# Optimization experiments

Hardware: AMD Instinct MI355X
Metric: run time of the kernel (lower is better)

The kernel has to match this reference:

```python
import jax, jax.numpy as jnp
import numpy as np

NUM_HEADS = 16


def setup_inputs() -> dict:
    key = jax.random.key(0)
    ks = jax.random.split(key, 4)
    B, C, T, D = 1, 1, 3072, 1024
    s = 1.0 / np.sqrt(D)
    return {
        "x": jax.random.normal(ks[0], (B, C, T, D), dtype=jnp.float32),
        "Wq": jax.random.normal(ks[1], (D, D), dtype=jnp.float32) * s,
        "bq": jnp.zeros((D,), dtype=jnp.float32),
        "Wk": jax.random.normal(ks[2], (D, D), dtype=jnp.float32) * s,
        "bk": jnp.zeros((D,), dtype=jnp.float32),
        "Wv": jax.random.normal(ks[3], (D, D), dtype=jnp.float32) * s,
        "bv": jnp.zeros((D,), dtype=jnp.float32),
        "gamma": jnp.float32(0.5),  # learned scalar; 0.0 at torch init, nonzero here for a meaningful signal
    }


def reference(x, Wq, bq, Wk, bk, Wv, bv, gamma):
    # x: (B, C, T, D); Linear acts on last dim (torch: y = x @ W.T + b)
    B, C, T, D = x.shape
    H = NUM_HEADS
    q = (jnp.einsum("bctd,ed->bcte", x, Wq) + bq).reshape(B, -1, T, H)  # (B, X, T, H), X = C*D/H
    k = (jnp.einsum("bctd,ed->bcte", x, Wk) + bk).reshape(B, -1, T, H)
    v = (jnp.einsum("bctd,ed->bcte", x, Wv) + bv).reshape(B, -1, T, H)
    q = q.transpose(0, 3, 2, 1)  # (B, H, T, X)
    k = k.transpose(0, 3, 1, 2)  # (B, H, X, T)
    energy = q @ k               # (B, H, T, T)  -- note: NO 1/sqrt(d) scaling, as in source
    attn = jax.nn.softmax(energy, axis=-1)
    v = v.transpose(0, 3, 2, 1)  # (B, H, T, X)
    out = attn @ v               # (B, H, T, X)
    out = out.transpose(0, 2, 3, 1).reshape(B, T, -1)  # (B, T, X*H) = (B, T, C*D)
    # residual broadcast: (B, T, C*D) + (B, C, T, D); valid since B == C == 1
    return gamma * out + x
```

## Files before the change

kernel.cpp:

```cpp
#include <hip/hip_runtime.h>


typedef _Float16 v8h __attribute__((ext_vector_type(8)));
typedef _Float16 v4h __attribute__((ext_vector_type(4)));
typedef __fp16   v2pk __attribute__((ext_vector_type(2)));
typedef __fp16   v4pk __attribute__((ext_vector_type(4)));
typedef float    v4f __attribute__((ext_vector_type(4)));

#define TSEQ 3072
#define DM   1024
#define NH   16
#define XD   64
#define LOG2E 1.44269504f

__device__ __forceinline__ void async_load16(const void* g, void* l) {
  __builtin_amdgcn_global_load_lds(
      (const __attribute__((address_space(1))) unsigned int*)g,
      (__attribute__((address_space(3))) unsigned int*)l,
      16, 0, 0);
}

__device__ __forceinline__ float fexp2(float x) {
  float r; asm("v_exp_f32 %0, %1" : "=v"(r) : "v"(x)); return r;
}
__device__ __forceinline__ float flog2(float x) {
  float r; asm("v_log_f32 %0, %1" : "=v"(r) : "v"(x)); return r;
}

extern "C" __global__ __launch_bounds__(256) void cvt_kernel(
    const float* __restrict__ x, const float* __restrict__ wq,
    const float* __restrict__ wk, const float* __restrict__ wv,
    _Float16* __restrict__ xb, _Float16* __restrict__ wb)
{
  const int NX4 = (TSEQ * DM) / 4;
  const int NT  = NX4 * 2;
  for (int i = blockIdx.x * blockDim.x + threadIdx.x; i < NT;
       i += gridDim.x * blockDim.x) {
    float4 v;
    _Float16* dst;
    if (i < NX4) {
      v = ((const float4*)x)[i];
      dst = xb + (size_t)i * 4;
    } else {
      const int j = i - NX4;
      const int n = j >> 8;
      if (n < 1024)      v = ((const float4*)wq)[j];
      else if (n < 2048) v = ((const float4*)wk)[j - 262144];
      else               v = ((const float4*)wv)[j - 524288];
      dst = wb + (size_t)j * 4;
    }
    v4h h;
    h[0] = (_Float16)v.x; h[1] = (_Float16)v.y;
    h[2] = (_Float16)v.z; h[3] = (_Float16)v.w;
    *(v4h*)dst = h;
  }
}

extern "C" __global__ __launch_bounds__(256) void qkv_gemm_kernel(
    const _Float16* __restrict__ xb, const _Float16* __restrict__ wb,
    const float* __restrict__ bq, const float* __restrict__ bk,
    const float* __restrict__ bv,
    _Float16* __restrict__ qlin, _Float16* __restrict__ klin,
    _Float16* __restrict__ vlin)
{
  __shared__ _Float16 As[128 * 32];
  __shared__ _Float16 Bs[128 * 32];
  const int tid = threadIdx.x;
  const int w = tid >> 6, l = tid & 63;
  const int li = l & 15, lg = l >> 4;
  const int wm = w >> 1, wn = w & 1;
  const int bid = blockIdx.x;
  const int swz = (bid & 7) * 72 + (bid >> 3);
  const int m0 = (swz / 24) * 128, n0 = (swz % 24) * 128;
  v4f acc[4][4] = {};
  const int srow = l >> 2;
  const int scol = (l & 3) * 8;
  for (int k0 = 0; k0 < DM; k0 += 32) {
#pragma unroll
    for (int c = 0; c < 2; ++c) {
      const int rbase = c * 64 + w * 16;
      async_load16(xb + (size_t)(m0 + rbase + srow) * DM + k0 + scol, &As[rbase * 32]);
      async_load16(wb + (size_t)(n0 + rbase + srow) * DM + k0 + scol, &Bs[rbase * 32]);
    }
    __syncthreads();
    v8h af[4], bf[4];
#pragma unroll
    for (int mi = 0; mi < 4; ++mi)
      af[mi] = *(const v8h*)&As[(wm * 64 + mi * 16 + li) * 32 + lg * 8];
#pragma unroll
    for (int ni = 0; ni < 4; ++ni)
      bf[ni] = *(const v8h*)&Bs[(wn * 64 + ni * 16 + li) * 32 + lg * 8];
#pragma unroll
    for (int mi = 0; mi < 4; ++mi)
#pragma unroll
      for (int ni = 0; ni < 4; ++ni)
        acc[mi][ni] = __builtin_amdgcn_mfma_f32_16x16x32_f16(
            af[mi], bf[ni], acc[mi][ni], 0, 0, 0);
    __syncthreads();
  }
  const int which = n0 >> 10;
  const int ebase = n0 & 1023;
  const float* bias = which == 0 ? bq : (which == 1 ? bk : bv);
  _Float16* outp = which == 0 ? qlin : (which == 1 ? klin : vlin);
#pragma unroll
  for (int mi = 0; mi < 4; ++mi)
#pragma unroll
    for (int r = 0; r < 4; ++r) {
      const int t = m0 + wm * 64 + mi * 16 + lg * 4 + r;
#pragma unroll
      for (int ni = 0; ni < 4; ++ni) {
        const int e = ebase + wn * 64 + ni * 16 + li;
        outp[(size_t)t * DM + e] = (_Float16)(acc[mi][ni][r] + bias[e]);
      }
    }
}

extern "C" __global__ __launch_bounds__(256) void repack_kernel(
    const _Float16* __restrict__ qlin, const _Float16* __restrict__ klin,
    const _Float16* __restrict__ vlin,
    _Float16* __restrict__ qh, _Float16* __restrict__ kh,
    _Float16* __restrict__ vt)
{
  const int NE = NH * TSEQ * XD;
  for (int g = blockIdx.x * blockDim.x + threadIdx.x; g < 3 * NE;
       g += gridDim.x * blockDim.x) {
    if (g < 2 * NE) {
      const int gg = (g < NE) ? g : g - NE;
      const int xx = gg & 63;
      const int rest = gg >> 6;
      const int h = rest / TSEQ;
      const int i = rest - h * TSEQ;
      const int t = xx * 48 + (i >> 6);
      const int e = ((i & 63) << 4) + h;
      if (g < NE) qh[gg] = qlin[t * DM + e];
      else        kh[gg] = (_Float16)((float)klin[t * DM + e] * LOG2E);
    } else {
      const int o = g - 2 * NE;
      const int j = o % TSEQ;
      const int rest = o / TSEQ;
      const int xx = rest & 63;
      const int h = rest >> 6;
      const int t = xx * 48 + (j >> 6);
      const int e = ((j & 63) << 4) + h;
      vt[o] = vlin[t * DM + e];
    }
  }
}

extern "C" __global__ __launch_bounds__(256) void attn_kernel(
    const _Float16* __restrict__ qh, const _Float16* __restrict__ kh,
    const _Float16* __restrict__ vt, _Float16* __restrict__ pOut)
{
  __shared__ _Float16 Ks[2][4096];
  __shared__ _Float16 Vs[2][4096];
  __shared__ float sml[64];
  const int tid = threadIdx.x;
  const int w = tid >> 6, l = tid & 63;
  const int li = l & 15, lg = l >> 4;
  const int rw = w & 1, g = w >> 1;
  const int b = blockIdx.x;
  const int q = b >> 3;
  const int head = (b & 7) + ((q >= 48) ? 8 : 0);
  const int i0 = (q - ((q >= 48) ? 48 : 0)) * 64;
  const size_t hb = (size_t)head * TSEQ * XD;

  v8h qf[2][2];
#pragma unroll
  for (int ct = 0; ct < 2; ++ct) {
    const _Float16* qrow = qh + hb + (size_t)(i0 + rw * 32 + ct * 16 + li) * XD;
    qf[ct][0] = *(const v8h*)(qrow + lg * 8);
    qf[ct][1] = *(const v8h*)(qrow + 32 + lg * 8);
  }
  float m2[2] = {24.0f * LOG2E, 24.0f * LOG2E};
  float l4[2] = {0.0f, 0.0f};
  v4f oacc[4][2] = {};
  const int r8 = l >> 3, c8 = l & 7;

  for (int j0 = 0; j0 < TSEQ; j0 += 128) {
    const int jt = j0 + g * 64;
#pragma unroll
    for (int s = 0; s < 4; ++s) {
      const int n = rw * 4 + s;
      const int row = n * 8 + r8;
      async_load16(kh + hb + (size_t)(jt + row) * XD + ((c8 ^ (row & 7)) * 8),
                   &Ks[g][n * 512]);
      async_load16(vt + hb + (size_t)row * TSEQ + jt + ((c8 ^ (row & 7)) * 8),
                   &Vs[g][n * 512]);
    }
    __syncthreads();

    v4f e4[2][4];
#pragma unroll
    for (int kt = 0; kt < 4; ++kt) {
      const int krow = kt * 16 + li;
      const v8h kf0 = *(const v8h*)&Ks[g][krow * 64 + ((lg ^ (li & 7)) * 8)];
      const v8h kf1 = *(const v8h*)&Ks[g][krow * 64 + (((4 + lg) ^ (li & 7)) * 8)];
#pragma unroll
      for (int ct = 0; ct < 2; ++ct) {
        v4f a = {-m2[ct], -m2[ct], -m2[ct], -m2[ct]};
        a = __builtin_amdgcn_mfma_f32_16x16x32_f16(kf0, qf[ct][0], a, 0, 0, 0);
        a = __builtin_amdgcn_mfma_f32_16x16x32_f16(kf1, qf[ct][1], a, 0, 0, 0);
        e4[ct][kt] = a;
      }
    }

    float gm = -1.0e30f;
#pragma unroll
    for (int ct = 0; ct < 2; ++ct)
#pragma unroll
      for (int kt = 0; kt < 4; ++kt)
        gm = fmaxf(fmaxf(gm, fmaxf(e4[ct][kt][0], e4[ct][kt][1])),
                   fmaxf(e4[ct][kt][2], e4[ct][kt][3]));
    if (__any(gm > 11.5f)) {
#pragma unroll
      for (int ct = 0; ct < 2; ++ct) {
        float rm = -1.0e30f;
#pragma unroll
        for (int kt = 0; kt < 4; ++kt)
          rm = fmaxf(fmaxf(rm, fmaxf(e4[ct][kt][0], e4[ct][kt][1])),
                     fmaxf(e4[ct][kt][2], e4[ct][kt][3]));
        rm = fmaxf(rm, __shfl_xor(rm, 16, 64));
        rm = fmaxf(rm, __shfl_xor(rm, 32, 64));
        rm = fmaxf(rm, 0.0f);
        const float fs = fexp2(-rm);
#pragma unroll
        for (int kt = 0; kt < 4; ++kt)
#pragma unroll
          for (int r = 0; r < 4; ++r) e4[ct][kt][r] -= rm;
        l4[ct] *= fs;
#pragma unroll
        for (int mi = 0; mi < 4; ++mi) oacc[mi][ct] *= fs;
        m2[ct] += rm;
      }
    }

    v4h pv[2][4];
#pragma unroll
    for (int ct = 0; ct < 2; ++ct) {
#pragma unroll
      for (int kt = 0; kt < 4; ++kt) {
        const float p0 = fexp2(e4[ct][kt][0]);
        const float p1 = fexp2(e4[ct][kt][1]);
        const float p2 = fexp2(e4[ct][kt][2]);
        const float p3 = fexp2(e4[ct][kt][3]);
        const v2pk lo = __builtin_amdgcn_cvt_pkrtz(p0, p1);
        const v2pk hi = __builtin_amdgcn_cvt_pkrtz(p2, p3);
        const v4pk pk = __builtin_shufflevector(lo, hi, 0, 1, 2, 3);
        pv[ct][kt] = __builtin_bit_cast(v4h, pk);
        l4[ct] += (p0 + p1) + (p2 + p3);
      }
    }

#pragma unroll
    for (int mi = 0; mi < 4; ++mi) {
      const int vrow = mi * 16 + li;
      const int vb = vrow * 64 + (lg & 1) * 4;
#pragma unroll
      for (int kt = 0; kt < 4; ++kt) {
        const v4h vf = *(const v4h*)&Vs[g][vb + (((kt * 2 + (lg >> 1)) ^ (li & 7)) * 8)];
#pragma unroll
        for (int ct = 0; ct < 2; ++ct)
          oacc[mi][ct] = __builtin_amdgcn_mfma_f32_16x16x16f16(
              vf, pv[ct][kt], oacc[mi][ct], 0, 0, 0);
      }
    }
    __syncthreads();
  }

  float sv[2], inv[2];
#pragma unroll
  for (int ct = 0; ct < 2; ++ct) {
    float ls = l4[ct];
    ls += __shfl_xor(ls, 16, 64);
    ls += __shfl_xor(ls, 32, 64);
    inv[ct] = 1.0f / ls;
    sv[ct] = m2[ct] + flog2(ls);
  }
  _Float16* mb = &Ks[0][0];
  if (g == 1) {
#pragma unroll
    for (int ct = 0; ct < 2; ++ct) {
      const int rl = rw * 32 + ct * 16 + li;
      if (lg == 0) sml[rl] = sv[ct];
#pragma unroll
      for (int mi = 0; mi < 4; ++mi) {
        v4h o4;
#pragma unroll
        for (int r = 0; r < 4; ++r) o4[r] = (_Float16)(oacc[mi][ct][r] * inv[ct]);
        *(v4h*)&mb[rl * 64 + mi * 16 + lg * 4] = o4;
      }
    }
  }
  __syncthreads();
  if (g == 0) {
#pragma unroll
    for (int ct = 0; ct < 2; ++ct) {
      const int rl = rw * 32 + ct * 16 + li;
      const float s1 = sml[rl];
      const float M = fmaxf(sv[ct], s1);
      const float u0 = fexp2(sv[ct] - M), u1 = fexp2(s1 - M);
      const float den = 1.0f / (u0 + u1);
      const float c0 = u0 * den * inv[ct], c1 = u1 * den;
#pragma unroll
      for (int mi = 0; mi < 4; ++mi) {
        const v4h o1 = *(const v4h*)&mb[rl * 64 + mi * 16 + lg * 4];
        v4h o4;
#pragma unroll
        for (int r = 0; r < 4; ++r)
          o4[r] = (_Float16)(c0 * oacc[mi][ct][r] + c1 * (float)o1[r]);
        *(v4h*)&pOut[(size_t)(i0 + rl) * DM + head * 64 + mi * 16 + lg * 4] = o4;
      }
    }
  }
}

extern "C" __global__ __launch_bounds__(256) void epilogue_kernel(
    const _Float16* __restrict__ pO, const float* __restrict__ xin,
    const float* __restrict__ gscal, float* __restrict__ outp)
{
  __shared__ _Float16 po[8 * 1024];
  const int tid = threadIdx.x;
  const size_t t0 = (size_t)blockIdx.x * 8;
  {
    const _Float16* src = pO + t0 * DM + tid * 32;
    v8h* d = (v8h*)&po[tid * 32];
#pragma unroll
    for (int c = 0; c < 4; ++c) d[c] = *(const v8h*)(src + c * 8);
  }
  __syncthreads();
  const float g = gscal[0];
  const int tr = tid >> 5;
  const int d0 = (tid & 31) * 32;
  const size_t rb = (t0 + tr) * DM + d0;
#pragma unroll
  for (int c4 = 0; c4 < 8; ++c4) {
    const float4 xi = *(const float4*)&xin[rb + c4 * 4];
    float4 r;
    r.x = g * (float)po[tr * 1024 + ((c4 * 4 + 0) & 15) * 64 + ((d0 + c4 * 4 + 0) >> 4)] + xi.x;
    r.y = g * (float)po[tr * 1024 + ((c4 * 4 + 1) & 15) * 64 + ((d0 + c4 * 4 + 1) >> 4)] + xi.y;
    r.z = g * (float)po[tr * 1024 + ((c4 * 4 + 2) & 15) * 64 + ((d0 + c4 * 4 + 2) >> 4)] + xi.z;
    r.w = g * (float)po[tr * 1024 + ((c4 * 4 + 3) & 15) * 64 + ((d0 + c4 * 4 + 3) >> 4)] + xi.w;
    *(float4*)&outp[rb + c4 * 4] = r;
  }
}

extern "C" void kernel_launch(void* const* d_in, const int* in_sizes, int n_in,
                              void* d_out, int out_size, void* d_ws, size_t ws_size,
                              hipStream_t stream)
{
  const float* x  = (const float*)d_in[0];
  const float* Wq = (const float*)d_in[1];
  const float* bq = (const float*)d_in[2];
  const float* Wk = (const float*)d_in[3];
  const float* bk = (const float*)d_in[4];
  const float* Wv = (const float*)d_in[5];
  const float* bv = (const float*)d_in[6];
  const float* gm = (const float*)d_in[7];
  float* outp = (float*)d_out;
  char* ws = (char*)d_ws;
  const size_t SZH = (size_t)TSEQ * DM * sizeof(_Float16);
  _Float16* xb   = (_Float16*)(ws);
  _Float16* wb   = (_Float16*)(ws + SZH);
  _Float16* qlin = (_Float16*)(ws + 2 * SZH);
  _Float16* klin = (_Float16*)(ws + 3 * SZH);
  _Float16* vlin = (_Float16*)(ws + 4 * SZH);
  _Float16* qhp  = (_Float16*)(ws + 5 * SZH);
  _Float16* khp  = (_Float16*)(ws + 6 * SZH);
  _Float16* vtp  = (_Float16*)(ws + 7 * SZH);
  _Float16* pO   = (_Float16*)(ws);

  cvt_kernel<<<dim3(1024), dim3(256), 0, stream>>>(x, Wq, Wk, Wv, xb, wb);
  qkv_gemm_kernel<<<dim3(576), dim3(256), 0, stream>>>(xb, wb, bq, bk, bv,
                                                       qlin, klin, vlin);
  repack_kernel<<<dim3(4096), dim3(256), 0, stream>>>(qlin, klin, vlin,
                                                      qhp, khp, vtp);
  attn_kernel<<<dim3(768), dim3(256), 0, stream>>>(qhp, khp, vtp, pO);
  epilogue_kernel<<<dim3(384), dim3(256), 0, stream>>>(pO, x, gm, outp);
  (void)in_sizes; (void)n_in; (void)out_size; (void)ws_size;
}
```

Measured before the change: 152.2 us.

## Double-buffer K/V tiles in LDS and raise wave priority around MFMA blocks

Doubles the shared K and V tile buffers so the next tile's async global-to-LDS loads are issued before computing the current tile. A partial vmcnt wait replaces the full sync, which overlaps memory latency with the QK and PV MFMA work. It also raises wave priority with s_setprio around the MFMA sections. The cost is twice the LDS footprint (64 KB), which may reduce occupancy, and it relies on a hand-counted vmcnt value.

```diff
diff --git a/kernel.cpp b/kernel.cpp
--- a/kernel.cpp
+++ b/kernel.cpp
@@ -151,8 +151,8 @@
     const _Float16* __restrict__ qh, const _Float16* __restrict__ kh,
     const _Float16* __restrict__ vt, _Float16* __restrict__ pOut)
 {
-  __shared__ _Float16 Ks[2][4096];
-  __shared__ _Float16 Vs[2][4096];
+  __shared__ _Float16 Ks[2][2][4096];
+  __shared__ _Float16 Vs[2][2][4096];
   __shared__ float sml[64];
   const int tid = threadIdx.x;
   const int w = tid >> 6, l = tid & 63;
@@ -176,25 +176,41 @@
   v4f oacc[4][2] = {};
   const int r8 = l >> 3, c8 = l & 7;
 
-  for (int j0 = 0; j0 < TSEQ; j0 += 128) {
-    const int jt = j0 + g * 64;
+  auto stage = [&](int buf, int jt) {
 #pragma unroll
     for (int s = 0; s < 4; ++s) {
       const int n = rw * 4 + s;
       const int row = n * 8 + r8;
       async_load16(kh + hb + (size_t)(jt + row) * XD + ((c8 ^ (row & 7)) * 8),
-                   &Ks[g][n * 512]);
+                   &Ks[buf][g][n * 512]);
       async_load16(vt + hb + (size_t)row * TSEQ + jt + ((c8 ^ (row & 7)) * 8),
-                   &Vs[g][n * 512]);
-    }
-    __syncthreads();
+                   &Vs[buf][g][n * 512]);
+    }
+  };
+
+  const int NT = TSEQ / 128;
+  stage(0, g * 64);
+  for (int it = 0; it < NT; ++it) {
+    const int cur = it & 1;
+    if (it + 1 < NT) {
+      stage(cur ^ 1, (it + 1) * 128 + g * 64);
+      asm volatile("s_waitcnt vmcnt(8)" ::: "memory");
+    } else {
+      asm volatile("s_waitcnt vmcnt(0)" ::: "memory");
+    }
+    __builtin_amdgcn_sched_barrier(0);
+    __builtin_amdgcn_s_barrier();
+
+    const _Float16* Kc = &Ks[cur][g][0];
+    const _Float16* Vc = &Vs[cur][g][0];
 
     v4f e4[2][4];
+    __builtin_amdgcn_s_setprio(1);
 #pragma unroll
     for (int kt = 0; kt < 4; ++kt) {
       const int krow = kt * 16 + li;
-      const v8h kf0 = *(const v8h*)&Ks[g][krow * 64 + ((lg ^ (li & 7)) * 8)];
-      const v8h kf1 = *(const v8h*)&Ks[g][krow * 64 + (((4 + lg) ^ (li & 7)) * 8)];
+      const v8h kf0 = *(const v8h*)&Kc[krow * 64 + ((lg ^ (li & 7)) * 8)];
+      const v8h kf1 = *(const v8h*)&Kc[krow * 64 + (((4 + lg) ^ (li & 7)) * 8)];
 #pragma unroll
       for (int ct = 0; ct < 2; ++ct) {
         v4f a = {-m2[ct], -m2[ct], -m2[ct], -m2[ct]};
@@ -203,6 +219,7 @@
         e4[ct][kt] = a;
       }
     }
+    __builtin_amdgcn_s_setprio(0);
 
     float gm = -1.0e30f;
 #pragma unroll
@@ -251,20 +268,23 @@
       }
     }
 
+    __builtin_amdgcn_s_setprio(1);
 #pragma unroll
     for (int mi = 0; mi < 4; ++mi) {
       const int vrow = mi * 16 + li;
       const int vb = vrow * 64 + (lg & 1) * 4;
 #pragma unroll
       for (int kt = 0; kt < 4; ++kt) {
-        const v4h vf = *(const v4h*)&Vs[g][vb + (((kt * 2 + (lg >> 1)) ^ (li & 7)) * 8)];
+        const v4h vf = *(const v4h*)&Vc[vb + (((kt * 2 + (lg >> 1)) ^ (li & 7)) * 8)];
 #pragma unroll
         for (int ct = 0; ct < 2; ++ct)
           oacc[mi][ct] = __builtin_amdgcn_mfma_f32_16x16x16f16(
               vf, pv[ct][kt], oacc[mi][ct], 0, 0, 0);
       }
     }
-    __syncthreads();
+    __builtin_amdgcn_s_setprio(0);
+    __builtin_amdgcn_sched_barrier(0);
+    __builtin_amdgcn_s_barrier();
   }
 
   float sv[2], inv[2];
@@ -276,7 +296,7 @@
     inv[ct] = 1.0f / ls;
     sv[ct] = m2[ct] + flog2(ls);
   }
-  _Float16* mb = &Ks[0][0];
+  _Float16* mb = &Ks[0][0][0];
   if (g == 1) {
 #pragma unroll
     for (int ct = 0; ct < 2; ++ct) {
```

New measurement: 156.6 us. +2.9%, slower.
